# Optimization experiments

Measured on AMD Instinct MI355X. Metric: run time of the kernel, lower is better.

Reference implementation:

```python
import jax, jax.numpy as jnp
import numpy as np

_B, _H, _W = 4, 352, 1216
_N = 400000
_CIN, _CHID, _COUT = 64, 16, 64
_EPS = 1e-5


def setup_inputs() -> dict:
    key = jax.random.key(0)
    ks = jax.random.split(key, 12)
    pc_features = jax.random.normal(ks[0], (_N, _CIN), dtype=jnp.float32)
    # Pinhole intrinsics, identical per batch image (KITTI-like)
    fx = fy = 500.0
    cx, cy = _W / 2.0, _H / 2.0
    K0 = jnp.array([[fx, 0.0, cx], [0.0, fy, cy], [0.0, 0.0, 1.0]], dtype=jnp.float32)
    cam = jnp.tile(K0[None], (_B, 1, 1))
    # Sample uniform pixel coords + depth, back-project so projection is uniform over the image
    u = jax.random.uniform(ks[1], (_N,), minval=0.0, maxval=_W - 1.0)
    v = jax.random.uniform(ks[2], (_N,), minval=0.0, maxval=_H - 1.0)
    z = jax.random.uniform(ks[3], (_N,), minval=1.0, maxval=50.0)
    x = (u - cx) * z / fx
    y = (v - cy) * z / fy
    pc_pos = jnp.stack([x, y, z], axis=-1).astype(jnp.float32)
    pc_batch = jax.random.randint(ks[4], (_N,), 0, _B, dtype=jnp.int32)
    # MLP([64, 16, 64]) params
    W1 = jax.random.normal(ks[5], (_CIN, _CHID), dtype=jnp.float32) / np.sqrt(_CIN)
    b1 = jnp.zeros((_CHID,), dtype=jnp.float32)
    W2 = jax.random.normal(ks[6], (_CHID, _COUT), dtype=jnp.float32) / np.sqrt(_CHID)
    b2 = jnp.zeros((_COUT,), dtype=jnp.float32)
    zero_encoding = 0.02 * jax.random.normal(ks[7], (1, _COUT), dtype=jnp.float32)
    gamma = jnp.ones((_COUT,), dtype=jnp.float32)
    beta = jnp.zeros((_COUT,), dtype=jnp.float32)
    return {
        'pc_features': pc_features, 'pc_pos': pc_pos, 'pc_batch': pc_batch, 'cam': cam,
        'W1': W1, 'b1': b1, 'W2': W2, 'b2': b2, 'zero_encoding': zero_encoding,
        'gamma': gamma, 'beta': beta, 'B': _B, 'H': _H, 'W': _W,
    }


def reference(pc_features, pc_pos, pc_batch, cam, W1, b1, W2, b2, zero_encoding, gamma, beta, B, H, W):
    # MLP projection of per-point features: 64 -> 16 -> 64
    feats = jax.nn.relu(pc_features @ W1 + b1) @ W2 + b2  # [N, C]
    C = feats.shape[1]
    # project_pc: pinhole projection of points into the image grid
    Kp = cam[pc_batch]                                    # [N, 3, 3]
    p = jnp.einsum('nij,nj->ni', Kp, pc_pos)              # [N, 3]
    u = p[:, 0] / p[:, 2]
    v = p[:, 1] / p[:, 2]
    ui = jnp.clip(jnp.floor(u), 0, W - 1).astype(jnp.int32)
    vi = jnp.clip(jnp.floor(v), 0, H - 1).astype(jnp.int32)
    flat_idx = pc_batch * (H * W) + vi * W + ui           # [N]
    # Grid initialized with learned zero_encoding (pixels without points keep it),
    # then point features scattered at their projected pixel locations.
    grid = jnp.broadcast_to(zero_encoding, (B * H * W, C))
    grid = grid.at[flat_idx].set(feats)
    grid = grid.reshape(B, H, W, C).transpose(0, 3, 1, 2)  # [B, C, H, W]
    # BatchNorm2d (training mode: batch statistics over B,H,W)
    mean = grid.mean(axis=(0, 2, 3), keepdims=True)
    var = grid.var(axis=(0, 2, 3), keepdims=True)
    out = (grid - mean) * jax.lax.rsqrt(var + _EPS)
    out = out * gamma.reshape(1, -1, 1, 1) + beta.reshape(1, -1, 1, 1)
    return out
```

## Files before the change

kernel.cpp:

```cpp
#include <hip/hip_runtime.h>
#include <math.h>

#define TPB   256
#define CIN   64
#define CHID  16
#define COUT  64
#define BB    4
#define HH    352
#define WW    1216
#define HW_   (HH * WW)
#define MTOT  (BB * HW_)
#define NCOPY 32
#define WTILES (WW / 64)


__global__ __launch_bounds__(TPB) void k_init(int* __restrict__ winner,
                                              float* __restrict__ statsf,
                                              int* __restrict__ count) {
    int i = blockIdx.x * TPB + threadIdx.x;
    if (i < MTOT) winner[i] = -1;
    if (i < NCOPY * 128) statsf[i] = 0.0f;
    if (i == 0) *count = 0;
}

__global__ __launch_bounds__(TPB) void k_project(const float* __restrict__ pos,
                                                 const int* __restrict__ batch,
                                                 const float* __restrict__ cam,
                                                 int N,
                                                 int* __restrict__ winner,
                                                 int* __restrict__ pixarr) {
    int n = blockIdx.x * TPB + threadIdx.x;
    if (n >= N) return;
    int b = batch[n];
    const float* Km = cam + b * 9;
    float x = pos[3 * n + 0];
    float y = pos[3 * n + 1];
    float z = pos[3 * n + 2];
    float p0 = __fadd_rn(__fadd_rn(__fmul_rn(Km[0], x), __fmul_rn(Km[1], y)),
                         __fmul_rn(Km[2], z));
    float p1 = __fadd_rn(__fadd_rn(__fmul_rn(Km[3], x), __fmul_rn(Km[4], y)),
                         __fmul_rn(Km[5], z));
    float p2 = __fadd_rn(__fadd_rn(__fmul_rn(Km[6], x), __fmul_rn(Km[7], y)),
                         __fmul_rn(Km[8], z));
    float u = __fdiv_rn(p0, p2);
    float v = __fdiv_rn(p1, p2);
    float uf = fminf(fmaxf(floorf(u), 0.0f), (float)(WW - 1));
    float vf = fminf(fmaxf(floorf(v), 0.0f), (float)(HH - 1));
    int ui = (int)uf;
    int vi = (int)vf;
    int p = b * HW_ + vi * WW + ui;
    pixarr[n] = p;
    atomicMax(&winner[p], n);
}

__global__ __launch_bounds__(TPB) void k_stats(const float* __restrict__ feat,
        const float* __restrict__ W1, const float* __restrict__ b1,
        const float* __restrict__ W2, const float* __restrict__ b2,
        const int* __restrict__ winner, const int* __restrict__ pixarr,
        int N, float* __restrict__ statsf, int* __restrict__ count) {
    __shared__ float W1s[CIN * CHID];
    __shared__ float W2s[CHID * COUT];
    __shared__ float b1s[CHID];
    __shared__ float b2s[COUT];
    __shared__ float hid_s[TPB * 17];
    __shared__ float act_s[TPB];

    int t = threadIdx.x;
    for (int i = t; i < CIN * CHID; i += TPB) W1s[i] = W1[i];
    for (int i = t; i < CHID * COUT; i += TPB) W2s[i] = W2[i];
    if (t < CHID) b1s[t] = b1[t];
    if (t < COUT) b2s[t] = b2[t];
    __syncthreads();

    int n = blockIdx.x * TPB + t;
    bool active = false;
    if (n < N) active = (winner[pixarr[n]] == n);

    unsigned long long mb = __ballot(active);
    if ((t & 63) == 0) atomicAdd(count, (int)__popcll(mb));

    float hloc[CHID];
#pragma unroll
    for (int h = 0; h < CHID; h++) hloc[h] = 0.0f;
    if (active) {
#pragma unroll
        for (int h = 0; h < CHID; h++) hloc[h] = b1s[h];
        const float4* X = (const float4*)(feat + (size_t)n * CIN);
#pragma unroll
        for (int j = 0; j < 16; j++) {
            float4 x4 = X[j];
            const float* w = &W1s[4 * j * CHID];
#pragma unroll
            for (int h = 0; h < CHID; h++) {
                float acc = hloc[h];
                acc = fmaf(x4.x, w[h], acc);
                acc = fmaf(x4.y, w[CHID + h], acc);
                acc = fmaf(x4.z, w[2 * CHID + h], acc);
                acc = fmaf(x4.w, w[3 * CHID + h], acc);
                hloc[h] = acc;
            }
        }
#pragma unroll
        for (int h = 0; h < CHID; h++) hloc[h] = fmaxf(hloc[h], 0.0f);
    }
#pragma unroll
    for (int h = 0; h < CHID; h++) hid_s[t * 17 + h] = hloc[h];
    act_s[t] = active ? 1.0f : 0.0f;
    __syncthreads();

    int c = t & 63;
    int g = t >> 6;
    float s = 0.0f, q = 0.0f;
    for (int i = 0; i < 64; i++) {
        int p = g * 64 + i;
        float a = act_s[p];
        float f = b2s[c];
#pragma unroll
        for (int h = 0; h < CHID; h++)
            f = fmaf(hid_s[p * 17 + h], W2s[h * COUT + c], f);
        float fa = f * a;
        s += fa;
        q = fmaf(fa, f, q);
    }
    float* dst = statsf + (blockIdx.x & (NCOPY - 1)) * 128;
    atomicAdd(&dst[c], s);
    atomicAdd(&dst[64 + c], q);
}

__global__ __launch_bounds__(TPB) void k_out(const float* __restrict__ feat,
        const float* __restrict__ W1, const float* __restrict__ b1,
        const float* __restrict__ W2, const float* __restrict__ b2,
        const float* __restrict__ zenc, const float* __restrict__ gmm,
        const float* __restrict__ bta, const int* __restrict__ winner,
        const float* __restrict__ statsf, const int* __restrict__ count,
        float* __restrict__ out) {
    __shared__ float W1s[CIN * CHID];
    __shared__ float W2s[CHID * COUT];
    __shared__ float b1s[CHID];
    __shared__ float b2s[COUT];
    __shared__ float scale_s[COUT], shift_s[COUT], empty_s[COUT];
    __shared__ float hid_s[64 * 17];
    __shared__ int   n_s[64];

    int t = threadIdx.x;
    int blk = blockIdx.x;
    int wt = blk % WTILES;
    int hh = (blk / WTILES) % HH;
    int bb = blk / (WTILES * HH);
    int w0 = wt * 64;
    int pix0 = bb * HW_ + hh * WW + w0;

    for (int i = t; i < CIN * CHID; i += TPB) W1s[i] = W1[i];
    for (int i = t; i < CHID * COUT; i += TPB) W2s[i] = W2[i];
    if (t < CHID) b1s[t] = b1[t];
    if (t < COUT) b2s[t] = b2[t];
    if (t < 64) {
        float s = 0.0f, q = 0.0f;
        for (int g = 0; g < NCOPY; g++) {
            s += statsf[g * 128 + t];
            q += statsf[g * 128 + 64 + t];
        }
        float Kc = (float)(*count);
        const float Mf = (float)MTOT;
        float zc = zenc[t];
        float mean = (s + (Mf - Kc) * zc) / Mf;
        float e2   = (q + (Mf - Kc) * zc * zc) / Mf;
        float var  = e2 - mean * mean;
        float inv  = 1.0f / sqrtf(var + 1e-5f);
        float sc = gmm[t] * inv;
        float sh = bta[t] - mean * sc;
        scale_s[t] = sc;
        shift_s[t] = sh;
        empty_s[t] = fmaf(zc, sc, sh);
        n_s[t] = winner[pix0 + t];
    }
    __syncthreads();

    {
        int p  = t & 63;
        int h0 = (t >> 6) * 4;
        int n  = n_s[p];
        float a0 = 0.0f, a1 = 0.0f, a2 = 0.0f, a3 = 0.0f;
        if (n >= 0) {
            a0 = b1s[h0]; a1 = b1s[h0 + 1]; a2 = b1s[h0 + 2]; a3 = b1s[h0 + 3];
            const float4* X = (const float4*)(feat + (size_t)n * CIN);
#pragma unroll
            for (int j = 0; j < 16; j++) {
                float4 x4 = X[j];
                const float* w = &W1s[4 * j * CHID + h0];
                a0 = fmaf(x4.x, w[0], a0);
                a1 = fmaf(x4.x, w[1], a1);
                a2 = fmaf(x4.x, w[2], a2);
                a3 = fmaf(x4.x, w[3], a3);
                a0 = fmaf(x4.y, w[CHID + 0], a0);
                a1 = fmaf(x4.y, w[CHID + 1], a1);
                a2 = fmaf(x4.y, w[CHID + 2], a2);
                a3 = fmaf(x4.y, w[CHID + 3], a3);
                a0 = fmaf(x4.z, w[2 * CHID + 0], a0);
                a1 = fmaf(x4.z, w[2 * CHID + 1], a1);
                a2 = fmaf(x4.z, w[2 * CHID + 2], a2);
                a3 = fmaf(x4.z, w[2 * CHID + 3], a3);
                a0 = fmaf(x4.w, w[3 * CHID + 0], a0);
                a1 = fmaf(x4.w, w[3 * CHID + 1], a1);
                a2 = fmaf(x4.w, w[3 * CHID + 2], a2);
                a3 = fmaf(x4.w, w[3 * CHID + 3], a3);
            }
            a0 = fmaxf(a0, 0.0f);
            a1 = fmaxf(a1, 0.0f);
            a2 = fmaxf(a2, 0.0f);
            a3 = fmaxf(a3, 0.0f);
        }
        hid_s[p * 17 + h0 + 0] = a0;
        hid_s[p * 17 + h0 + 1] = a1;
        hid_s[p * 17 + h0 + 2] = a2;
        hid_s[p * 17 + h0 + 3] = a3;
    }
    __syncthreads();

    {
        int p  = t & 63;
        int c0 = t >> 6;
        int n  = n_s[p];
        float hr[CHID];
#pragma unroll
        for (int h = 0; h < CHID; h++) hr[h] = hid_s[p * 17 + h];
        size_t ob = (((size_t)bb * COUT) * HH + hh) * (size_t)WW + w0 + p;
#pragma unroll
        for (int k = 0; k < 16; k++) {
            int c = c0 + 4 * k;
            float val;
            if (n >= 0) {
                float f = b2s[c];
#pragma unroll
                for (int h = 0; h < CHID; h++)
                    f = fmaf(hr[h], W2s[h * COUT + c], f);
                val = fmaf(f, scale_s[c], shift_s[c]);
            } else {
                val = empty_s[c];
            }
            out[ob + (size_t)c * HW_] = val;
        }
    }
}

extern "C" void kernel_launch(void* const* d_in, const int* in_sizes, int n_in,
                              void* d_out, int out_size, void* d_ws, size_t ws_size,
                              hipStream_t stream) {
    const float* feat  = (const float*)d_in[0];
    const float* pos   = (const float*)d_in[1];
    const int*   batch = (const int*)d_in[2];
    const float* cam   = (const float*)d_in[3];
    const float* W1    = (const float*)d_in[4];
    const float* b1    = (const float*)d_in[5];
    const float* W2    = (const float*)d_in[6];
    const float* b2    = (const float*)d_in[7];
    const float* zenc  = (const float*)d_in[8];
    const float* gmm   = (const float*)d_in[9];
    const float* bta   = (const float*)d_in[10];
    int N = in_sizes[2];

    int*   winner = (int*)d_ws;
    int*   pixarr = winner + MTOT;
    float* statsf = (float*)(pixarr + N);
    int*   count  = (int*)(statsf + NCOPY * 128);
    float* outp   = (float*)d_out;

    k_init<<<(MTOT + TPB - 1) / TPB, TPB, 0, stream>>>(winner, statsf, count);
    k_project<<<(N + TPB - 1) / TPB, TPB, 0, stream>>>(pos, batch, cam, N, winner, pixarr);
    k_stats<<<(N + TPB - 1) / TPB, TPB, 0, stream>>>(feat, W1, b1, W2, b2,
                                                     winner, pixarr, N, statsf, count);
    k_out<<<BB * HH * WTILES, TPB, 0, stream>>>(feat, W1, b1, W2, b2, zenc, gmm, bta,
                                                winner, statsf, count, outp);
}
```

Baseline: 759.9 us.

## Materialize hidden activations once and fold BN scale into W2 for output pass

Computes the 16-wide hidden layer once per winning point and stores it to a workspace buffer, instead of recomputing the 64->16 matmul in both the stats and output kernels. A separate wave-per-chunk kernel accumulates bias-free sums and sums of squares, and a tiny finalize kernel folds the batch-norm scale and shift into a transposed W2 and a bias vector. The output kernel then reads 16 hidden floats per pixel and does a 16-wide dot product per channel, with one wave per 64-pixel tile. The init kernel now writes int4/float4. The cost is an extra N×16 float buffer plus two more kernel launches, and the sums kernel walks sequential rows per wave, which may give poor coalescing.

```diff
diff --git a/kernel.cpp b/kernel.cpp
--- a/kernel.cpp
+++ b/kernel.cpp
@@ -12,15 +12,17 @@
 #define MTOT  (BB * HW_)
 #define NCOPY 32
 #define WTILES (WW / 64)
-
-
-__global__ __launch_bounds__(TPB) void k_init(int* __restrict__ winner,
-                                              float* __restrict__ statsf,
+#define NTILES (BB * HH * WTILES)
+#define KS_BLOCKS 768
+
+
+__global__ __launch_bounds__(TPB) void k_init(int4* __restrict__ winner4,
+                                              float4* __restrict__ statsf4,
                                               int* __restrict__ count) {
-    int i = blockIdx.x * TPB + threadIdx.x;
-    if (i < MTOT) winner[i] = -1;
-    if (i < NCOPY * 128) statsf[i] = 0.0f;
-    if (i == 0) *count = 0;
+    int g = blockIdx.x * TPB + threadIdx.x;
+    if (g < MTOT / 4) winner4[g] = make_int4(-1, -1, -1, -1);
+    if (g < (NCOPY * 128) / 4) statsf4[g] = make_float4(0.f, 0.f, 0.f, 0.f);
+    if (g == 0) *count = 0;
 }
 
 __global__ __launch_bounds__(TPB) void k_project(const float* __restrict__ pos,
@@ -53,193 +55,149 @@
     atomicMax(&winner[p], n);
 }
 
-__global__ __launch_bounds__(TPB) void k_stats(const float* __restrict__ feat,
+__global__ __launch_bounds__(TPB) void k_hid(const float* __restrict__ feat,
         const float* __restrict__ W1, const float* __restrict__ b1,
-        const float* __restrict__ W2, const float* __restrict__ b2,
         const int* __restrict__ winner, const int* __restrict__ pixarr,
-        int N, float* __restrict__ statsf, int* __restrict__ count) {
-    __shared__ float W1s[CIN * CHID];
-    __shared__ float W2s[CHID * COUT];
-    __shared__ float b1s[CHID];
-    __shared__ float b2s[COUT];
-    __shared__ float hid_s[TPB * 17];
-    __shared__ float act_s[TPB];
-
-    int t = threadIdx.x;
-    for (int i = t; i < CIN * CHID; i += TPB) W1s[i] = W1[i];
-    for (int i = t; i < CHID * COUT; i += TPB) W2s[i] = W2[i];
-    if (t < CHID) b1s[t] = b1[t];
-    if (t < COUT) b2s[t] = b2[t];
-    __syncthreads();
-
-    int n = blockIdx.x * TPB + t;
-    bool active = false;
-    if (n < N) active = (winner[pixarr[n]] == n);
-
+        int N, float* __restrict__ hidw, int* __restrict__ count) {
+    int n = blockIdx.x * TPB + threadIdx.x;
+    if (n >= N) return;
+    bool active = (winner[pixarr[n]] == n);
     unsigned long long mb = __ballot(active);
-    if ((t & 63) == 0) atomicAdd(count, (int)__popcll(mb));
-
-    float hloc[CHID];
-#pragma unroll
-    for (int h = 0; h < CHID; h++) hloc[h] = 0.0f;
-    if (active) {
-#pragma unroll
-        for (int h = 0; h < CHID; h++) hloc[h] = b1s[h];
-        const float4* X = (const float4*)(feat + (size_t)n * CIN);
-#pragma unroll
-        for (int j = 0; j < 16; j++) {
-            float4 x4 = X[j];
-            const float* w = &W1s[4 * j * CHID];
-#pragma unroll
-            for (int h = 0; h < CHID; h++) {
-                float acc = hloc[h];
-                acc = fmaf(x4.x, w[h], acc);
-                acc = fmaf(x4.y, w[CHID + h], acc);
-                acc = fmaf(x4.z, w[2 * CHID + h], acc);
-                acc = fmaf(x4.w, w[3 * CHID + h], acc);
-                hloc[h] = acc;
+    if ((threadIdx.x & 63) == 0) atomicAdd(count, (int)__popcll(mb));
+
+    float h[CHID];
+#pragma unroll
+    for (int k = 0; k < CHID; k++) h[k] = b1[k];
+    const float4* X = (const float4*)(feat + (size_t)n * CIN);
+    const float4* W14 = (const float4*)W1;
+#pragma unroll
+    for (int j4 = 0; j4 < 16; j4++) {
+        float4 x4 = X[j4];
+#pragma unroll
+        for (int e = 0; e < 4; e++) {
+            int j = 4 * j4 + e;
+            float xj = (e == 0) ? x4.x : (e == 1) ? x4.y : (e == 2) ? x4.z : x4.w;
+#pragma unroll
+            for (int m = 0; m < 4; m++) {
+                float4 w = W14[j * 4 + m];
+                h[4 * m + 0] = fmaf(xj, w.x, h[4 * m + 0]);
+                h[4 * m + 1] = fmaf(xj, w.y, h[4 * m + 1]);
+                h[4 * m + 2] = fmaf(xj, w.z, h[4 * m + 2]);
+                h[4 * m + 3] = fmaf(xj, w.w, h[4 * m + 3]);
             }
         }
-#pragma unroll
-        for (int h = 0; h < CHID; h++) hloc[h] = fmaxf(hloc[h], 0.0f);
-    }
-#pragma unroll
-    for (int h = 0; h < CHID; h++) hid_s[t * 17 + h] = hloc[h];
-    act_s[t] = active ? 1.0f : 0.0f;
-    __syncthreads();
-
-    int c = t & 63;
-    int g = t >> 6;
-    float s = 0.0f, q = 0.0f;
-    for (int i = 0; i < 64; i++) {
-        int p = g * 64 + i;
-        float a = act_s[p];
-        float f = b2s[c];
-#pragma unroll
-        for (int h = 0; h < CHID; h++)
-            f = fmaf(hid_s[p * 17 + h], W2s[h * COUT + c], f);
-        float fa = f * a;
-        s += fa;
-        q = fmaf(fa, f, q);
-    }
-    float* dst = statsf + (blockIdx.x & (NCOPY - 1)) * 128;
+    }
+    float4* Ho = (float4*)(hidw + (size_t)n * CHID);
+#pragma unroll
+    for (int m = 0; m < 4; m++) {
+        float4 o;
+        o.x = active ? fmaxf(h[4 * m + 0], 0.f) : 0.f;
+        o.y = active ? fmaxf(h[4 * m + 1], 0.f) : 0.f;
+        o.z = active ? fmaxf(h[4 * m + 2], 0.f) : 0.f;
+        o.w = active ? fmaxf(h[4 * m + 3], 0.f) : 0.f;
+        Ho[m] = o;
+    }
+}
+
+__global__ __launch_bounds__(TPB) void k_sums(const float* __restrict__ hidw,
+        const float* __restrict__ W2, int N, float* __restrict__ statsf) {
+    int c = threadIdx.x & 63;
+    int wv = blockIdx.x * (TPB / 64) + (threadIdx.x >> 6);
+    wv = __builtin_amdgcn_readfirstlane(wv);
+    float w2c[CHID];
+#pragma unroll
+    for (int h = 0; h < CHID; h++) w2c[h] = W2[h * COUT + c];
+    const int TW = KS_BLOCKS * (TPB / 64);
+    int chunk = (N + TW - 1) / TW;
+    int i0 = wv * chunk;
+    int i1 = min(N, i0 + chunk);
+    float s = 0.f, q = 0.f;
+    for (int i = i0; i < i1; i++) {
+        const float4* Hp = (const float4*)(hidw + (size_t)i * CHID);
+        float g = 0.f;
+#pragma unroll
+        for (int m = 0; m < 4; m++) {
+            float4 hv = Hp[m];
+            g = fmaf(hv.x, w2c[4 * m + 0], g);
+            g = fmaf(hv.y, w2c[4 * m + 1], g);
+            g = fmaf(hv.z, w2c[4 * m + 2], g);
+            g = fmaf(hv.w, w2c[4 * m + 3], g);
+        }
+        s += g;
+        q = fmaf(g, g, q);
+    }
+    float* dst = statsf + (wv & (NCOPY - 1)) * 128;
     atomicAdd(&dst[c], s);
     atomicAdd(&dst[64 + c], q);
 }
 
-__global__ __launch_bounds__(TPB) void k_out(const float* __restrict__ feat,
-        const float* __restrict__ W1, const float* __restrict__ b1,
-        const float* __restrict__ W2, const float* __restrict__ b2,
-        const float* __restrict__ zenc, const float* __restrict__ gmm,
-        const float* __restrict__ bta, const int* __restrict__ winner,
-        const float* __restrict__ statsf, const int* __restrict__ count,
+__global__ __launch_bounds__(64) void k_finalize(const float* __restrict__ statsf,
+        const int* __restrict__ count, const float* __restrict__ W2,
+        const float* __restrict__ b2, const float* __restrict__ zenc,
+        const float* __restrict__ gmm, const float* __restrict__ bta,
+        float* __restrict__ w2tp, float* __restrict__ biasp,
+        float* __restrict__ emptyv) {
+    int c = threadIdx.x;
+    float S1 = 0.f, S2 = 0.f;
+    for (int g = 0; g < NCOPY; g++) {
+        S1 += statsf[g * 128 + c];
+        S2 += statsf[g * 128 + 64 + c];
+    }
+    float K = (float)(*count);
+    float b2c = b2[c];
+    float sumf  = K * b2c + S1;
+    float sumsq = fmaf(K * b2c, b2c, fmaf(2.f * b2c, S1, S2));
+    const float Mf = (float)MTOT;
+    float zc = zenc[c];
+    float mean = (sumf + (Mf - K) * zc) / Mf;
+    float e2   = (sumsq + (Mf - K) * zc * zc) / Mf;
+    float var  = e2 - mean * mean;
+    float inv  = 1.0f / sqrtf(var + 1e-5f);
+    float sc = gmm[c] * inv;
+    float sh = bta[c] - mean * sc;
+    emptyv[c] = fmaf(zc, sc, sh);
+    biasp[c]  = fmaf(b2c, sc, sh);
+    for (int h = 0; h < CHID; h++) w2tp[c * CHID + h] = W2[h * COUT + c] * sc;
+}
+
+__global__ __launch_bounds__(TPB) void k_out(const float* __restrict__ hidw,
+        const int* __restrict__ winner, const float* __restrict__ w2tp,
+        const float* __restrict__ biasp, const float* __restrict__ emptyv,
         float* __restrict__ out) {
-    __shared__ float W1s[CIN * CHID];
-    __shared__ float W2s[CHID * COUT];
-    __shared__ float b1s[CHID];
-    __shared__ float b2s[COUT];
-    __shared__ float scale_s[COUT], shift_s[COUT], empty_s[COUT];
-    __shared__ float hid_s[64 * 17];
-    __shared__ int   n_s[64];
-
-    int t = threadIdx.x;
-    int blk = blockIdx.x;
-    int wt = blk % WTILES;
-    int hh = (blk / WTILES) % HH;
-    int bb = blk / (WTILES * HH);
-    int w0 = wt * 64;
-    int pix0 = bb * HW_ + hh * WW + w0;
-
-    for (int i = t; i < CIN * CHID; i += TPB) W1s[i] = W1[i];
-    for (int i = t; i < CHID * COUT; i += TPB) W2s[i] = W2[i];
-    if (t < CHID) b1s[t] = b1[t];
-    if (t < COUT) b2s[t] = b2[t];
-    if (t < 64) {
-        float s = 0.0f, q = 0.0f;
-        for (int g = 0; g < NCOPY; g++) {
-            s += statsf[g * 128 + t];
-            q += statsf[g * 128 + 64 + t];
-        }
-        float Kc = (float)(*count);
-        const float Mf = (float)MTOT;
-        float zc = zenc[t];
-        float mean = (s + (Mf - Kc) * zc) / Mf;
-        float e2   = (q + (Mf - Kc) * zc * zc) / Mf;
-        float var  = e2 - mean * mean;
-        float inv  = 1.0f / sqrtf(var + 1e-5f);
-        float sc = gmm[t] * inv;
-        float sh = bta[t] - mean * sc;
-        scale_s[t] = sc;
-        shift_s[t] = sh;
-        empty_s[t] = fmaf(zc, sc, sh);
-        n_s[t] = winner[pix0 + t];
-    }
-    __syncthreads();
-
-    {
-        int p  = t & 63;
-        int h0 = (t >> 6) * 4;
-        int n  = n_s[p];
-        float a0 = 0.0f, a1 = 0.0f, a2 = 0.0f, a3 = 0.0f;
-        if (n >= 0) {
-            a0 = b1s[h0]; a1 = b1s[h0 + 1]; a2 = b1s[h0 + 2]; a3 = b1s[h0 + 3];
-            const float4* X = (const float4*)(feat + (size_t)n * CIN);
-#pragma unroll
-            for (int j = 0; j < 16; j++) {
-                float4 x4 = X[j];
-                const float* w = &W1s[4 * j * CHID + h0];
-                a0 = fmaf(x4.x, w[0], a0);
-                a1 = fmaf(x4.x, w[1], a1);
-                a2 = fmaf(x4.x, w[2], a2);
-                a3 = fmaf(x4.x, w[3], a3);
-                a0 = fmaf(x4.y, w[CHID + 0], a0);
-                a1 = fmaf(x4.y, w[CHID + 1], a1);
-                a2 = fmaf(x4.y, w[CHID + 2], a2);
-                a3 = fmaf(x4.y, w[CHID + 3], a3);
-                a0 = fmaf(x4.z, w[2 * CHID + 0], a0);
-                a1 = fmaf(x4.z, w[2 * CHID + 1], a1);
-                a2 = fmaf(x4.z, w[2 * CHID + 2], a2);
-                a3 = fmaf(x4.z, w[2 * CHID + 3], a3);
-                a0 = fmaf(x4.w, w[3 * CHID + 0], a0);
-                a1 = fmaf(x4.w, w[3 * CHID + 1], a1);
-                a2 = fmaf(x4.w, w[3 * CHID + 2], a2);
-                a3 = fmaf(x4.w, w[3 * CHID + 3], a3);
-            }
-            a0 = fmaxf(a0, 0.0f);
-            a1 = fmaxf(a1, 0.0f);
-            a2 = fmaxf(a2, 0.0f);
-            a3 = fmaxf(a3, 0.0f);
-        }
-        hid_s[p * 17 + h0 + 0] = a0;
-        hid_s[p * 17 + h0 + 1] = a1;
-        hid_s[p * 17 + h0 + 2] = a2;
-        hid_s[p * 17 + h0 + 3] = a3;
-    }
-    __syncthreads();
-
-    {
-        int p  = t & 63;
-        int c0 = t >> 6;
-        int n  = n_s[p];
-        float hr[CHID];
-#pragma unroll
-        for (int h = 0; h < CHID; h++) hr[h] = hid_s[p * 17 + h];
-        size_t ob = (((size_t)bb * COUT) * HH + hh) * (size_t)WW + w0 + p;
-#pragma unroll
-        for (int k = 0; k < 16; k++) {
-            int c = c0 + 4 * k;
-            float val;
-            if (n >= 0) {
-                float f = b2s[c];
-#pragma unroll
-                for (int h = 0; h < CHID; h++)
-                    f = fmaf(hr[h], W2s[h * COUT + c], f);
-                val = fmaf(f, scale_s[c], shift_s[c]);
-            } else {
-                val = empty_s[c];
-            }
-            out[ob + (size_t)c * HW_] = val;
-        }
+    int tile = blockIdx.x * (TPB / 64) + (threadIdx.x >> 6);
+    tile = __builtin_amdgcn_readfirstlane(tile);
+    int p = threadIdx.x & 63;
+    int wt  = tile % WTILES;
+    int rem = tile / WTILES;
+    int hh  = rem % HH;
+    int bb  = rem / HH;
+    int pix0 = bb * HW_ + hh * WW + wt * 64;
+
+    int n = winner[pix0 + p];
+    bool act = (n >= 0);
+    size_t nn = act ? (size_t)n : 0;
+    const float4* Hp = (const float4*)(hidw + nn * CHID);
+    float4 h0 = Hp[0], h1 = Hp[1], h2 = Hp[2], h3 = Hp[3];
+
+    float* ob = out + (size_t)bb * ((size_t)COUT * HW_) + (size_t)hh * WW + wt * 64 + p;
+    const float4* W4 = (const float4*)w2tp;
+#pragma unroll 4
+    for (int c = 0; c < COUT; c++) {
+        float4 wa = W4[c * 4 + 0];
+        float4 wb = W4[c * 4 + 1];
+        float4 wc = W4[c * 4 + 2];
+        float4 wd = W4[c * 4 + 3];
+        float f = biasp[c];
+        f = fmaf(h0.x, wa.x, f); f = fmaf(h0.y, wa.y, f);
+        f = fmaf(h0.z, wa.z, f); f = fmaf(h0.w, wa.w, f);
+        f = fmaf(h1.x, wb.x, f); f = fmaf(h1.y, wb.y, f);
+        f = fmaf(h1.z, wb.z, f); f = fmaf(h1.w, wb.w, f);
+        f = fmaf(h2.x, wc.x, f); f = fmaf(h2.y, wc.y, f);
+        f = fmaf(h2.z, wc.z, f); f = fmaf(h2.w, wc.w, f);
+        f = fmaf(h3.x, wd.x, f); f = fmaf(h3.y, wd.y, f);
+        f = fmaf(h3.z, wd.z, f); f = fmaf(h3.w, wd.w, f);
+        float ev = emptyv[c];
+        ob[(size_t)c * HW_] = act ? f : ev;
     }
 }
 
@@ -262,13 +220,19 @@
     int*   winner = (int*)d_ws;
     int*   pixarr = winner + MTOT;
     float* statsf = (float*)(pixarr + N);
-    int*   count  = (int*)(statsf + NCOPY * 128);
+    int*   misc   = (int*)(statsf + NCOPY * 128);
+    float* hidw   = (float*)(misc + 4);
+    float* w2tp   = hidw + (size_t)N * CHID;
+    float* biasp  = w2tp + COUT * CHID;
+    float* emptyv = biasp + COUT;
+    int*   count  = misc;
     float* outp   = (float*)d_out;
 
-    k_init<<<(MTOT + TPB - 1) / TPB, TPB, 0, stream>>>(winner, statsf, count);
+    k_init<<<MTOT / 4 / TPB, TPB, 0, stream>>>((int4*)winner, (float4*)statsf, count);
     k_project<<<(N + TPB - 1) / TPB, TPB, 0, stream>>>(pos, batch, cam, N, winner, pixarr);
-    k_stats<<<(N + TPB - 1) / TPB, TPB, 0, stream>>>(feat, W1, b1, W2, b2,
-                                                     winner, pixarr, N, statsf, count);
-    k_out<<<BB * HH * WTILES, TPB, 0, stream>>>(feat, W1, b1, W2, b2, zenc, gmm, bta,
-                                                winner, statsf, count, outp);
-}
+    k_hid<<<(N + TPB - 1) / TPB, TPB, 0, stream>>>(feat, W1, b1, winner, pixarr, N, hidw, count);
+    k_sums<<<KS_BLOCKS, TPB, 0, stream>>>(hidw, W2, N, statsf);
+    k_finalize<<<1, 64, 0, stream>>>(statsf, count, W2, b2, zenc, gmm, bta,
+                                     w2tp, biasp, emptyv);
+    k_out<<<NTILES / (TPB / 64), TPB, 0, stream>>>(hidw, winner, w2tp, biasp, emptyv, outp);
+}
```

Result: faster. 676.1 us (-11.0%).
